# Performance work log

Measured on AMD Instinct MI355X. Metric: run time of the kernel, lower is better.

Reference implementation:

```python
import jax, jax.numpy as jnp
import numpy as np

K = 3
PAD = 1


def conv2d(x, w, b, pad):
    y = jax.lax.conv_general_dilated(
        x, w, window_strides=(1, 1), padding=[(pad, pad), (pad, pad)],
        dimension_numbers=("NCHW", "OIHW", "NCHW"))
    return y + b[None, :, None, None]


def dcn_v2(f, w_off, b_off, w, b):
    # Modulated deformable conv (DCNv2), stride=1, pad=1, dilation=1, dg=1.
    B, C, H, W = f.shape
    om = conv2d(f, w_off, b_off, PAD)                 # [B, 27, H, W]
    o1, o2, m = jnp.split(om, 3, axis=1)
    offset = jnp.concatenate([o1, o2], axis=1).reshape(B, K * K, 2, H, W)
    dy, dx = offset[:, :, 0], offset[:, :, 1]          # [B, 9, H, W]
    mask = jax.nn.sigmoid(m)                           # [B, 9, H, W]
    ky = (jnp.arange(K * K) // K).astype(f.dtype)      # kernel row per tap
    kx = (jnp.arange(K * K) % K).astype(f.dtype)       # kernel col per tap
    hh = jnp.arange(H, dtype=f.dtype)
    ww = jnp.arange(W, dtype=f.dtype)
    ys = hh[None, None, :, None] - PAD + ky[None, :, None, None] + dy  # [B,9,H,W]
    xs = ww[None, None, None, :] - PAD + kx[None, :, None, None] + dx
    y0 = jnp.floor(ys)
    x0 = jnp.floor(xs)
    wy1 = ys - y0
    wx1 = xs - x0
    wy0 = 1.0 - wy1
    wx0 = 1.0 - wx1
    f_flat = f.reshape(B, C, H * W)

    def gather(yi, xi):
        valid = (yi >= 0) & (yi <= H - 1) & (xi >= 0) & (xi <= W - 1)
        yc = jnp.clip(yi, 0, H - 1).astype(jnp.int32)
        xc = jnp.clip(xi, 0, W - 1).astype(jnp.int32)
        idx = (yc * W + xc).reshape(B, 1, -1)          # [B,1,9*H*W]
        g = jnp.take_along_axis(f_flat, idx, axis=2).reshape(B, C, K * K, H, W)
        return g * valid.astype(f.dtype).reshape(B, 1, K * K, H, W)

    v = (gather(y0, x0) * (wy0 * wx0)[:, None]
         + gather(y0, x0 + 1) * (wy0 * wx1)[:, None]
         + gather(y0 + 1, x0) * (wy1 * wx0)[:, None]
         + gather(y0 + 1, x0 + 1) * (wy1 * wx1)[:, None])   # [B,C,9,H,W]
    v = v * mask[:, None]
    out = jnp.einsum("bckhw,ock->bohw", v, w.reshape(w.shape[0], C, K * K))
    return out + b[None, :, None, None]


def setup_inputs() -> dict:
    key = jax.random.key(0)
    ks = jax.random.split(key, 10)
    B, C, H, W = 2, 256, 128, 128
    s = 0.05
    return {
        "x": jax.random.normal(ks[0], (B, C, H, W), jnp.float32),
        "votes": jax.random.normal(ks[1], (B, C, H, W), jnp.float32),
        "w1": jax.random.normal(ks[2], (C, C, 3, 3), jnp.float32) * s,
        "b1": jnp.zeros((C,), jnp.float32),
        "w_off": jax.random.normal(ks[3], (27, C, 3, 3), jnp.float32) * 0.01,
        "b_off": jnp.zeros((27,), jnp.float32),
        "w_dcn": jax.random.normal(ks[4], (C, C, 3, 3), jnp.float32) * s,
        "b_dcn": jnp.zeros((C,), jnp.float32),
        "w2": jax.random.normal(ks[5], (C, C, 3, 3), jnp.float32) * s,
        "b2": jnp.zeros((C,), jnp.float32),
        "w3": jax.random.normal(ks[6], (C, C, 3, 3), jnp.float32) * s,
        "b3": jnp.zeros((C,), jnp.float32),
        "w4": jax.random.normal(ks[7], (2, C, 1, 1), jnp.float32) * s,
        "b4": jnp.zeros((2,), jnp.float32),
    }


def reference(x, votes, w1, b1, w_off, b_off, w_dcn, b_dcn, w2, b2, w3, b3, w4, b4):
    v = jax.nn.relu(votes)
    t = jax.nn.relu(conv2d(v, w1, b1, PAD))            # conv3x3 + relu
    t = jax.nn.relu(dcn_v2(t, w_off, b_off, w_dcn, b_dcn))  # DCN + relu
    t = conv2d(t, w2, b2, PAD)                         # conv3x3 (no relu)
    g = t * x                                          # gated by x
    h = jax.nn.relu(conv2d(g, w3, b3, PAD))            # conv3x3 + relu
    out = conv2d(h, w4, b4, 0)                         # 1x1 -> outplanes
    return out
```

## Files before the change

kernel.cpp:

```cpp
#include <hip/hip_runtime.h>
#include <math.h>

typedef short short8 __attribute__((ext_vector_type(8)));
typedef float f32x4 __attribute__((ext_vector_type(4)));
typedef unsigned int uint4v __attribute__((ext_vector_type(4)));
typedef unsigned short ushort_t;

__device__ inline ushort_t f2bf(float f) {
    unsigned u = __builtin_bit_cast(unsigned, f);
    u = (u + 0x7fffu + ((u >> 16) & 1u)) >> 16;
    return (ushort_t)u;
}
__device__ inline float bf2f(ushort_t u) {
    return __builtin_bit_cast(float, (unsigned)u << 16);
}
__device__ inline void gload_lds16(const ushort_t* g, short* l) {
    __builtin_amdgcn_global_load_lds((const __attribute__((address_space(1))) unsigned int*)g,
                                     (__attribute__((address_space(3))) unsigned int*)l, 16, 0, 0);
}

__global__ __launch_bounds__(256)
void zeroinit_kernel(ushort_t* zp) { zp[threadIdx.x] = 0; }

template<bool RELU>
__global__ __launch_bounds__(256)
void nhwc_cvt_kernel(const float* __restrict__ in, ushort_t* __restrict__ out) {
    __shared__ short s[64 * 66];
    const int tid = threadIdx.x;
    const int px0 = blockIdx.x * 64;
    const int ci0 = blockIdx.y * 64;
    const int b   = blockIdx.z;
    const float* inb = in + (size_t)b * 256 * 16384;
#pragma unroll
    for (int rep = 0; rep < 16; ++rep) {
        int cl = rep * 4 + (tid >> 6);
        int pl = tid & 63;
        float v = inb[(size_t)(ci0 + cl) * 16384 + px0 + pl];
        if (RELU) v = fmaxf(v, 0.f);
        s[pl * 66 + cl] = (short)f2bf(v);
    }
    __syncthreads();
    ushort_t* ob = out + (size_t)b * 16384 * 256;
#pragma unroll
    for (int rep = 0; rep < 2; ++rep) {
        int c = rep * 256 + tid;
        int pl = c >> 3;
        int cl = (c & 7) * 8;
        *(short8*)&ob[(size_t)(px0 + pl) * 256 + ci0 + cl] = *(const short8*)&s[pl * 66 + cl];
    }
}

__global__ __launch_bounds__(256)
void wpack_kernel(const float* __restrict__ w, ushort_t* __restrict__ wpk,
                  int COUT, int NF) {
    int T = blockIdx.x * 256 + threadIdx.x;
    int lane = T & 63;
    int rest = T >> 6;
    int n = rest % NF;
    int kstep = rest / NF;
    int t = kstep >> 3, cc = kstep & 7;
    int oc = n * 16 + (lane & 15);
    int kk = (lane >> 4) * 8;
    short8 sv;
#pragma unroll
    for (int j = 0; j < 8; ++j) {
        int ci = cc * 32 + kk + j;
        float val = (oc < COUT) ? w[((size_t)oc * 256 + ci) * 9 + t] : 0.f;
        sv[j] = (short)f2bf(val);
    }
    *(short8*)&wpk[(size_t)T * 8] = sv;
}

template<int OUTC, int EPI>
__global__ __launch_bounds__(512, 2)
void conv_mfma_kernel(const ushort_t* __restrict__ in, const ushort_t* __restrict__ wpk,
                      const float* __restrict__ bias, int coutReal,
                      const ushort_t* __restrict__ xin, ushort_t* __restrict__ outp,
                      const ushort_t* __restrict__ zp)
{
    constexpr int NF = OUTC / 16;
    constexpr int NN = (NF < 4) ? NF : 4;
    constexpr int PITCH = OUTC + 4;
    union SM { short a[2][256 * 32]; float e[32 * PITCH]; };
    __shared__ __align__(16) SM sm;

    const int tid  = threadIdx.x;
    const int lane = tid & 63;
    const int wv   = tid >> 6;
    const int hi   = lane >> 4;
    const int lo   = lane & 15;
    const int pxg  = wv & 1;
    const int wn   = wv >> 1;
    const int wnu  = __builtin_amdgcn_readfirstlane(wn);
    const int x0 = blockIdx.x * 32;
    const int y0 = blockIdx.y * 4;
    const int b  = blockIdx.z;
    const ushort_t* inb = in + (size_t)b * 16384 * 256;

    const ushort_t* sptr[2];
    int sstep[2];
#pragma unroll
    for (int r = 0; r < 2; ++r) {
        int g = r * 512 + tid;
        int px = g >> 2, slot = g & 3;
        int hy = px / 34, hx = px - hy * 34;
        int gy = y0 - 1 + hy, gx = x0 - 1 + hx;
        bool ok = (px < 204) && ((unsigned)gy < 128u) && ((unsigned)gx < 128u);
        int kk = (px ^ (px >> 2)) & 3;
        sptr[r] = ok ? (inb + (size_t)((gy << 7) + gx) * 256 + ((slot ^ kk) << 3))
                     : (zp + (slot << 3));
        sstep[r] = ok ? 32 : 0;
    }

    int pxh_base[4];
#pragma unroll
    for (int m = 0; m < 4; ++m)
        pxh_base[m] = (2 * pxg + (m >> 1)) * 34 + (m & 1) * 16 + lo;

    f32x4 acc[4][NN];
#pragma unroll
    for (int m = 0; m < 4; ++m)
#pragma unroll
        for (int n = 0; n < NN; ++n) acc[m][n] = (f32x4){0.f, 0.f, 0.f, 0.f};

#pragma unroll
    for (int r = 0; r < 2; ++r)
        gload_lds16(sptr[r], &sm.a[0][(r * 512 + wv * 64) * 8]);
    __syncthreads();

    for (int cc = 0; cc < 8; ++cc) {
        const int buf = cc & 1;
        if (cc < 7) {
#pragma unroll
            for (int r = 0; r < 2; ++r)
                gload_lds16(sptr[r] + (size_t)(cc + 1) * sstep[r],
                            &sm.a[buf ^ 1][(r * 512 + wv * 64) * 8]);
        }
        if (NF >= 4 || wnu == 0) {
#pragma unroll
            for (int t = 0; t < 9; ++t) {
                const int ky = t / 3, kx = t % 3;
                short8 bf[NN];
#pragma unroll
                for (int n = 0; n < NN; ++n)
                    bf[n] = *(const short8*)&wpk[((size_t)((t * 8 + cc) * NF + wnu * 4 + n) * 64 + lane) * 8];
                short8 af[4];
#pragma unroll
                for (int m = 0; m < 4; ++m) {
                    int ph = pxh_base[m] + ky * 34 + kx;
                    int off = ph * 32 + ((hi ^ ((ph ^ (ph >> 2)) & 3)) << 3);
                    af[m] = *(const short8*)&sm.a[buf][off];
                }
#pragma unroll
                for (int m = 0; m < 4; ++m)
#pragma unroll
                    for (int n = 0; n < NN; ++n)
                        acc[m][n] = __builtin_amdgcn_mfma_f32_16x16x32_bf16(af[m], bf[n], acc[m][n], 0, 0, 0);
            }
        }
        __syncthreads();
    }

    float br[NN];
#pragma unroll
    for (int n = 0; n < NN; ++n) {
        int oc = wn * 64 + n * 16 + lo;
        br[n] = (oc < coutReal) ? bias[oc] : 0.f;
    }
    const size_t obase = ((size_t)b * 16384 + (size_t)y0 * 128 + x0) * OUTC;
#pragma unroll
    for (int p = 0; p < 4; ++p) {
        if (pxg == (p >> 1) && (NF >= 4 || wnu == 0)) {
#pragma unroll
            for (int mm = 0; mm < 2; ++mm) {
                int m = (p & 1) * 2 + mm;
#pragma unroll
                for (int n = 0; n < NN; ++n)
#pragma unroll
                    for (int r = 0; r < 4; ++r) {
                        int col = mm * 16 + hi * 4 + r;
                        float v = acc[m][n][r] + br[n];
                        if (EPI == 1) v = fmaxf(v, 0.f);
                        sm.e[col * PITCH + wn * 64 + n * 16 + lo] = v;
                    }
            }
        }
        __syncthreads();
        constexpr int CHUNKS = 32 * OUTC / 8;
        for (int c = tid; c < CHUNKS; c += 512) {
            int col = c / (OUTC / 8);
            int ch = c % (OUTC / 8);
            f32x4 v0 = *(const f32x4*)&sm.e[col * PITCH + ch * 8];
            f32x4 v1 = *(const f32x4*)&sm.e[col * PITCH + ch * 8 + 4];
            size_t gidx = obase + ((size_t)p * 128 + col) * OUTC + ch * 8;
            if (EPI == 2) {
                uint4v xu = *(const uint4v*)&xin[gidx];
#pragma unroll
                for (int j = 0; j < 4; ++j) {
                    float xa = bf2f((ushort_t)(xu[j] & 0xffffu));
                    float xb = __builtin_bit_cast(float, xu[j] & 0xffff0000u);
                    if (j < 2) { v0[2 * j] *= xa; v0[2 * j + 1] *= xb; }
                    else       { v1[2 * (j - 2)] *= xa; v1[2 * (j - 2) + 1] *= xb; }
                }
            }
            short8 s;
#pragma unroll
            for (int j = 0; j < 4; ++j) s[j] = (short)f2bf(v0[j]);
#pragma unroll
            for (int j = 0; j < 4; ++j) s[4 + j] = (short)f2bf(v1[j]);
            *(short8*)&outp[gidx] = s;
        }
        __syncthreads();
    }
}

__device__ inline void corner8(uint4v u, float w, float* sv) {
#pragma unroll
    for (int j = 0; j < 4; ++j) {
        unsigned a = u[j];
        sv[2 * j]     = fmaf(w, __builtin_bit_cast(float, a << 16), sv[2 * j]);
        sv[2 * j + 1] = fmaf(w, __builtin_bit_cast(float, a & 0xffff0000u), sv[2 * j + 1]);
    }
}

__global__ __launch_bounds__(256, 2)
void dcn_mfma_kernel(const ushort_t* __restrict__ ft, const ushort_t* __restrict__ omt,
                     const ushort_t* __restrict__ wpk, const float* __restrict__ bias,
                     ushort_t* __restrict__ outp)
{
    union SM { short a[2][2][2048]; float e[16 * 264]; };
    __shared__ __align__(16) SM sm;

    const int tid  = threadIdx.x;
    const int lane = tid & 63;
    const int wv   = tid >> 6;
    const int hi   = lane >> 4;
    const int lo   = lane & 15;
    const int bid  = blockIdx.x;
    const int tile = (bid & 7) * 64 + (bid >> 3);
    const int b    = tile >> 8;
    const int rem  = tile & 255;
    const int y0   = (rem >> 3) * 4;
    const int x0   = (rem & 7) * 16;
    const ushort_t* fb = ft + (size_t)b * 16384 * 256;

    const int pxl = (wv << 4) | (lane >> 2);
    const int q   = lane & 3;

    float mw[9][4];
    unsigned mc[9];
    {
        const int py = y0 + (pxl >> 4), pxx = x0 + (pxl & 15);
        const ushort_t* omp = omt + ((size_t)b * 16384 + py * 128 + pxx) * 32;
        uint4v ow[4];
#pragma unroll
        for (int j = 0; j < 4; ++j) ow[j] = *(const uint4v*)(omp + j * 8);
        unsigned wbuf[14];
#pragma unroll
        for (int j = 0; j < 4; ++j)
#pragma unroll
            for (int e = 0; e < 4; ++e)
                if (j * 4 + e < 14) wbuf[j * 4 + e] = ow[j][e];
#pragma unroll
        for (int t = 0; t < 9; ++t) {
            float dy = bf2f((ushort_t)(wbuf[t] & 0xffffu));
            float dx = bf2f((ushort_t)(wbuf[t] >> 16));
            unsigned mw_ = wbuf[(18 + t) >> 1];
            float mr = ((18 + t) & 1) ? bf2f((ushort_t)(mw_ >> 16)) : bf2f((ushort_t)(mw_ & 0xffffu));
            float mk = 1.f / (1.f + expf(-mr));
            float ys = (float)(py - 1 + t / 3) + dy;
            float xs = (float)(pxx - 1 + t % 3) + dx;
            float y0f = floorf(ys), x0f = floorf(xs);
            float wy1 = ys - y0f, wx1 = xs - x0f;
            float wy0 = 1.f - wy1, wx0 = 1.f - wx1;
            int yi = (int)y0f, xi = (int)x0f;
            bool vy0 = (yi >= 0) && (yi < 128), vy1 = (yi + 1 >= 0) && (yi + 1 < 128);
            bool vx0 = (xi >= 0) && (xi < 128), vx1 = (xi + 1 >= 0) && (xi + 1 < 128);
            mw[t][0] = (vy0 && vx0) ? wy0 * wx0 * mk : 0.f;
            mw[t][1] = (vy0 && vx1) ? wy0 * wx1 * mk : 0.f;
            mw[t][2] = (vy1 && vx0) ? wy1 * wx0 * mk : 0.f;
            mw[t][3] = (vy1 && vx1) ? wy1 * wx1 * mk : 0.f;
            int y0c = min(max(yi, 0), 127), y1c = min(max(yi + 1, 0), 127);
            int x0c = min(max(xi, 0), 127), x1c = min(max(xi + 1, 0), 127);
            mc[t] = (unsigned)y0c | ((unsigned)y1c << 8) | ((unsigned)x0c << 16) | ((unsigned)x1c << 24);
        }
    }

    const int w_off = pxl * 32 + ((q ^ ((pxl ^ (pxl >> 2)) & 3)) << 3);
    int a_off[4];
#pragma unroll
    for (int m = 0; m < 4; ++m) {
        int p_ = m * 16 + lo;
        a_off[m] = p_ * 32 + ((hi ^ ((p_ ^ (p_ >> 2)) & 3)) << 3);
    }

    f32x4 acc[4][4];
#pragma unroll
    for (int m = 0; m < 4; ++m)
#pragma unroll
        for (int n = 0; n < 4; ++n) acc[m][n] = (f32x4){0.f, 0.f, 0.f, 0.f};

    uint4v n0a, n0b, n0c, n0d;
    uint4v n1a, n1b, n1c, n1d;

    {
        unsigned c = mc[0];
        int yy0 = c & 255, yy1 = (c >> 8) & 255, xx0 = (c >> 16) & 255, xx1 = c >> 24;
        size_t o00 = (size_t)((yy0 << 7) + xx0) * 256, o01 = (size_t)((yy0 << 7) + xx1) * 256;
        size_t o10 = (size_t)((yy1 << 7) + xx0) * 256, o11 = (size_t)((yy1 << 7) + xx1) * 256;
#pragma unroll
        for (int h = 0; h < 2; ++h) {
            const ushort_t* pc = fb + h * 32 + q * 8;
            uint4v g0 = *(const uint4v*)(pc + o00);
            uint4v g1 = *(const uint4v*)(pc + o01);
            uint4v g2 = *(const uint4v*)(pc + o10);
            uint4v g3 = *(const uint4v*)(pc + o11);
            float sv[8] = {0.f, 0.f, 0.f, 0.f, 0.f, 0.f, 0.f, 0.f};
            corner8(g0, mw[0][0], sv); corner8(g1, mw[0][1], sv);
            corner8(g2, mw[0][2], sv); corner8(g3, mw[0][3], sv);
            unsigned pk[4];
#pragma unroll
            for (int j = 0; j < 4; ++j)
                asm("v_cvt_pk_bf16_f32 %0, %1, %2" : "=v"(pk[j]) : "v"(sv[2 * j]), "v"(sv[2 * j + 1]));
            *(uint4v*)&sm.a[0][h][w_off] = (uint4v){pk[0], pk[1], pk[2], pk[3]};
        }
    }
    __syncthreads();

    for (int cch = 0; cch < 4; ++cch) {
#pragma unroll
        for (int t = 0; t < 9; ++t) {
            const int cur = (cch + t) & 1;
            const bool last = (cch == 3) && (t == 8);
            const int tn   = (t == 8) ? 0 : t + 1;
            const int cchn = (t == 8) ? cch + 1 : cch;
            if (!last) {
                unsigned c = mc[tn];
                int yy0 = c & 255, yy1 = (c >> 8) & 255, xx0 = (c >> 16) & 255, xx1 = c >> 24;
                size_t o00 = (size_t)((yy0 << 7) + xx0) * 256, o01 = (size_t)((yy0 << 7) + xx1) * 256;
                size_t o10 = (size_t)((yy1 << 7) + xx0) * 256, o11 = (size_t)((yy1 << 7) + xx1) * 256;
                const ushort_t* pc0 = fb + (2 * cchn) * 32 + q * 8;
                n0a = *(const uint4v*)(pc0 + o00);
                n0b = *(const uint4v*)(pc0 + o01);
                n0c = *(const uint4v*)(pc0 + o10);
                n0d = *(const uint4v*)(pc0 + o11);
                const ushort_t* pc1 = pc0 + 32;
                n1a = *(const uint4v*)(pc1 + o00);
                n1b = *(const uint4v*)(pc1 + o01);
                n1c = *(const uint4v*)(pc1 + o10);
                n1d = *(const uint4v*)(pc1 + o11);
            }
            short8 bfr0[4], bfr1[4];
            {
                const ushort_t* bs0 = wpk + ((size_t)((t * 8 + 2 * cch) * 16 + wv * 4) * 64 + lane) * 8;
#pragma unroll
                for (int n = 0; n < 4; ++n)
                    bfr0[n] = *(const short8*)(bs0 + (size_t)n * 512);
                const ushort_t* bs1 = bs0 + 16 * 512;
#pragma unroll
                for (int n = 0; n < 4; ++n)
                    bfr1[n] = *(const short8*)(bs1 + (size_t)n * 512);
            }
#pragma unroll
            for (int m = 0; m < 4; ++m) {
                short8 af0 = *(const short8*)&sm.a[cur][0][a_off[m]];
                short8 af1 = *(const short8*)&sm.a[cur][1][a_off[m]];
#pragma unroll
                for (int n = 0; n < 4; ++n)
                    acc[m][n] = __builtin_amdgcn_mfma_f32_16x16x32_bf16(af0, bfr0[n], acc[m][n], 0, 0, 0);
#pragma unroll
                for (int n = 0; n < 4; ++n)
                    acc[m][n] = __builtin_amdgcn_mfma_f32_16x16x32_bf16(af1, bfr1[n], acc[m][n], 0, 0, 0);
            }
            if (!last) {
                {
                    float sv[8] = {0.f, 0.f, 0.f, 0.f, 0.f, 0.f, 0.f, 0.f};
                    corner8(n0a, mw[tn][0], sv); corner8(n0b, mw[tn][1], sv);
                    corner8(n0c, mw[tn][2], sv); corner8(n0d, mw[tn][3], sv);
                    unsigned pk[4];
#pragma unroll
                    for (int j = 0; j < 4; ++j)
                        asm("v_cvt_pk_bf16_f32 %0, %1, %2" : "=v"(pk[j]) : "v"(sv[2 * j]), "v"(sv[2 * j + 1]));
                    *(uint4v*)&sm.a[cur ^ 1][0][w_off] = (uint4v){pk[0], pk[1], pk[2], pk[3]};
                }
                {
                    float sv[8] = {0.f, 0.f, 0.f, 0.f, 0.f, 0.f, 0.f, 0.f};
                    corner8(n1a, mw[tn][0], sv); corner8(n1b, mw[tn][1], sv);
                    corner8(n1c, mw[tn][2], sv); corner8(n1d, mw[tn][3], sv);
                    unsigned pk[4];
#pragma unroll
                    for (int j = 0; j < 4; ++j)
                        asm("v_cvt_pk_bf16_f32 %0, %1, %2" : "=v"(pk[j]) : "v"(sv[2 * j]), "v"(sv[2 * j + 1]));
                    *(uint4v*)&sm.a[cur ^ 1][1][w_off] = (uint4v){pk[0], pk[1], pk[2], pk[3]};
                }
            }
            __syncthreads();
        }
    }

    float br[4];
#pragma unroll
    for (int n = 0; n < 4; ++n) br[n] = bias[wv * 64 + n * 16 + lo];
#pragma unroll
    for (int p = 0; p < 4; ++p) {
#pragma unroll
        for (int n = 0; n < 4; ++n)
#pragma unroll
            for (int r = 0; r < 4; ++r)
                sm.e[(hi * 4 + r) * 264 + wv * 64 + n * 16 + lo] = fmaxf(acc[p][n][r] + br[n], 0.f);
        __syncthreads();
#pragma unroll
        for (int j = 0; j < 2; ++j) {
            int c2 = j * 256 + tid;
            int pl = c2 >> 5, ch = c2 & 31;
            f32x4 v0 = *(const f32x4*)&sm.e[pl * 264 + ch * 8];
            f32x4 v1 = *(const f32x4*)&sm.e[pl * 264 + ch * 8 + 4];
            short8 s;
#pragma unroll
            for (int jj = 0; jj < 4; ++jj) s[jj] = (short)f2bf(v0[jj]);
#pragma unroll
            for (int jj = 0; jj < 4; ++jj) s[4 + jj] = (short)f2bf(v1[jj]);
            *(short8*)&outp[((size_t)b * 16384 + (size_t)(y0 + p) * 128 + x0 + pl) * 256 + ch * 8] = s;
        }
        __syncthreads();
    }
}

__global__ __launch_bounds__(256)
void conv1x1_kernel(const ushort_t* __restrict__ in, const float* __restrict__ w,
                    const float* __restrict__ bias, float* __restrict__ out)
{
    __shared__ float sw[512];
    for (int i = threadIdx.x; i < 512; i += 256) sw[i] = w[i];
    __syncthreads();
    int px = blockIdx.x * 256 + threadIdx.x;
    int b = px >> 14, p = px & 16383;
    const ushort_t* ip = in + (size_t)px * 256;
    float a0 = 0.f, a1 = 0.f;
#pragma unroll
    for (int ch = 0; ch < 32; ++ch) {
        uint4v u = *(const uint4v*)&ip[ch * 8];
#pragma unroll
        for (int j = 0; j < 4; ++j) {
            int ci = ch * 8 + 2 * j;
            float fa = __builtin_bit_cast(float, u[j] << 16);
            float fb = __builtin_bit_cast(float, u[j] & 0xffff0000u);
            a0 = fmaf(fa, sw[ci], a0);      a1 = fmaf(fa, sw[256 + ci], a1);
            a0 = fmaf(fb, sw[ci + 1], a0);  a1 = fmaf(fb, sw[256 + ci + 1], a1);
        }
    }
    out[(size_t)b * 2 * 16384 + p]         = a0 + bias[0];
    out[(size_t)b * 2 * 16384 + 16384 + p] = a1 + bias[1];
}

extern "C" void kernel_launch(void* const* d_in, const int* in_sizes, int n_in,
                              void* d_out, int out_size, void* d_ws, size_t ws_size,
                              hipStream_t stream) {
    const float* x     = (const float*)d_in[0];
    const float* votes = (const float*)d_in[1];
    const float* w1    = (const float*)d_in[2];
    const float* b1    = (const float*)d_in[3];
    const float* w_off = (const float*)d_in[4];
    const float* b_off = (const float*)d_in[5];
    const float* w_dcn = (const float*)d_in[6];
    const float* b_dcn = (const float*)d_in[7];
    const float* w2    = (const float*)d_in[8];
    const float* b2    = (const float*)d_in[9];
    const float* w3    = (const float*)d_in[10];
    const float* b3    = (const float*)d_in[11];
    const float* w4    = (const float*)d_in[12];
    const float* b4    = (const float*)d_in[13];
    float* outp = (float*)d_out;

    const int B = 2;
    const size_t featN = (size_t)B * 16384 * 256;

    ushort_t* ws   = (ushort_t*)d_ws;
    ushort_t* t1   = ws;
    ushort_t* t2   = t1 + featN;
    ushort_t* aN   = t2 + featN;
    ushort_t* xN   = aN + featN;
    ushort_t* om   = xN + featN;
    ushort_t* wpk1 = om + (size_t)B * 16384 * 32;
    ushort_t* wpkO = wpk1 + 589824;
    ushort_t* wpkD = wpkO + 73728;
    ushort_t* wpk2 = wpkD + 589824;
    ushort_t* wpk3 = wpk2 + 589824;
    ushort_t* zp   = wpk3 + 589824;

    zeroinit_kernel<<<1, 256, 0, stream>>>(zp);
    nhwc_cvt_kernel<true><<<dim3(256, 4, B), 256, 0, stream>>>(votes, aN);
    nhwc_cvt_kernel<false><<<dim3(256, 4, B), 256, 0, stream>>>(x, xN);
    wpack_kernel<<<288, 256, 0, stream>>>(w1, wpk1, 256, 16);
    wpack_kernel<<<36, 256, 0, stream>>>(w_off, wpkO, 27, 2);
    wpack_kernel<<<288, 256, 0, stream>>>(w_dcn, wpkD, 256, 16);
    wpack_kernel<<<288, 256, 0, stream>>>(w2, wpk2, 256, 16);
    wpack_kernel<<<288, 256, 0, stream>>>(w3, wpk3, 256, 16);

    dim3 cg(4, 32, B);
    conv_mfma_kernel<256, 1><<<cg, 512, 0, stream>>>(aN, wpk1, b1, 256, nullptr, t1, zp);
    conv_mfma_kernel<32, 0><<<cg, 512, 0, stream>>>(t1, wpkO, b_off, 27, nullptr, om, zp);
    dcn_mfma_kernel<<<512, 256, 0, stream>>>(t1, om, wpkD, b_dcn, t2);
    conv_mfma_kernel<256, 2><<<cg, 512, 0, stream>>>(t2, wpk2, b2, 256, xN, aN, zp);
    conv_mfma_kernel<256, 1><<<cg, 512, 0, stream>>>(aN, wpk3, b3, 256, nullptr, xN, zp);
    conv1x1_kernel<<<128, 256, 0, stream>>>(xN, w4, b4, outp);
}
```

Baseline: 278.0 us.

## Split conv output channels across blocks and merge prep kernels

The 3x3 conv kernels now compute 128 output channels per block, with the channel half picked from blockIdx.z. This doubles the grid from 256 to 512 blocks and halves the accumulator count per wave (NN 4 to 2). The weight-pack, zero-init and NHWC conversion launches are merged into two kernels to cut launch overhead. In exchange, each input tile is loaded into LDS twice, once per channel half, and each block issues fewer MFMAs per A-fragment load.

```diff
diff --git a/kernel.cpp b/kernel.cpp
--- a/kernel.cpp
+++ b/kernel.cpp
@@ -19,41 +19,9 @@
                                      (__attribute__((address_space(3))) unsigned int*)l, 16, 0, 0);
 }
 
-__global__ __launch_bounds__(256)
-void zeroinit_kernel(ushort_t* zp) { zp[threadIdx.x] = 0; }
-
-template<bool RELU>
-__global__ __launch_bounds__(256)
-void nhwc_cvt_kernel(const float* __restrict__ in, ushort_t* __restrict__ out) {
-    __shared__ short s[64 * 66];
-    const int tid = threadIdx.x;
-    const int px0 = blockIdx.x * 64;
-    const int ci0 = blockIdx.y * 64;
-    const int b   = blockIdx.z;
-    const float* inb = in + (size_t)b * 256 * 16384;
-#pragma unroll
-    for (int rep = 0; rep < 16; ++rep) {
-        int cl = rep * 4 + (tid >> 6);
-        int pl = tid & 63;
-        float v = inb[(size_t)(ci0 + cl) * 16384 + px0 + pl];
-        if (RELU) v = fmaxf(v, 0.f);
-        s[pl * 66 + cl] = (short)f2bf(v);
-    }
-    __syncthreads();
-    ushort_t* ob = out + (size_t)b * 16384 * 256;
-#pragma unroll
-    for (int rep = 0; rep < 2; ++rep) {
-        int c = rep * 256 + tid;
-        int pl = c >> 3;
-        int cl = (c & 7) * 8;
-        *(short8*)&ob[(size_t)(px0 + pl) * 256 + ci0 + cl] = *(const short8*)&s[pl * 66 + cl];
-    }
-}
-
-__global__ __launch_bounds__(256)
-void wpack_kernel(const float* __restrict__ w, ushort_t* __restrict__ wpk,
-                  int COUT, int NF) {
-    int T = blockIdx.x * 256 + threadIdx.x;
+__device__ inline void wpack_body(const float* __restrict__ w, ushort_t* __restrict__ wpk,
+                                  int COUT, int NF, int bidLocal, int tid) {
+    int T = bidLocal * 256 + tid;
     int lane = T & 63;
     int rest = T >> 6;
     int n = rest % NF;
@@ -71,15 +39,61 @@
     *(short8*)&wpk[(size_t)T * 8] = sv;
 }
 
+__global__ __launch_bounds__(256)
+void wpack_all_kernel(const float* w1, ushort_t* wpk1,
+                      const float* w_off, ushort_t* wpkO,
+                      const float* w_dcn, ushort_t* wpkD,
+                      const float* w2, ushort_t* wpk2,
+                      const float* w3, ushort_t* wpk3,
+                      ushort_t* zp) {
+    int bid = blockIdx.x, tid = threadIdx.x;
+    if (bid < 288)       wpack_body(w1,    wpk1, 256, 16, bid,        tid);
+    else if (bid < 324)  wpack_body(w_off, wpkO, 27,  2,  bid - 288,  tid);
+    else if (bid < 612)  wpack_body(w_dcn, wpkD, 256, 16, bid - 324,  tid);
+    else if (bid < 900)  wpack_body(w2,    wpk2, 256, 16, bid - 612,  tid);
+    else if (bid < 1188) wpack_body(w3,    wpk3, 256, 16, bid - 900,  tid);
+    else                 zp[tid] = 0;
+}
+
+__global__ __launch_bounds__(256)
+void nhwc_all_kernel(const float* __restrict__ votes, const float* __restrict__ x,
+                     ushort_t* __restrict__ aN, ushort_t* __restrict__ xN) {
+    __shared__ short s[64 * 66];
+    const int tid = threadIdx.x;
+    const int px0 = blockIdx.x * 64;
+    const int ci0 = blockIdx.y * 64;
+    const int z   = blockIdx.z;
+    const int b   = z & 1;
+    const bool doRelu = (z < 2);
+    const float* inb = (doRelu ? votes : x) + (size_t)b * 256 * 16384;
+    ushort_t* ob = (doRelu ? aN : xN) + (size_t)b * 16384 * 256;
+#pragma unroll
+    for (int rep = 0; rep < 16; ++rep) {
+        int cl = rep * 4 + (tid >> 6);
+        int pl = tid & 63;
+        float v = inb[(size_t)(ci0 + cl) * 16384 + px0 + pl];
+        if (doRelu) v = fmaxf(v, 0.f);
+        s[pl * 66 + cl] = (short)f2bf(v);
+    }
+    __syncthreads();
+#pragma unroll
+    for (int rep = 0; rep < 2; ++rep) {
+        int c = rep * 256 + tid;
+        int pl = c >> 3;
+        int cl = (c & 7) * 8;
+        *(short8*)&ob[(size_t)(px0 + pl) * 256 + ci0 + cl] = *(const short8*)&s[pl * 66 + cl];
+    }
+}
+
 template<int OUTC, int EPI>
 __global__ __launch_bounds__(512, 2)
 void conv_mfma_kernel(const ushort_t* __restrict__ in, const ushort_t* __restrict__ wpk,
                       const float* __restrict__ bias, int coutReal,
                       const ushort_t* __restrict__ xin, ushort_t* __restrict__ outp,
-                      const ushort_t* __restrict__ zp)
+                      const ushort_t* __restrict__ zp, int nfTot, int nOcBlk, int ocStr)
 {
     constexpr int NF = OUTC / 16;
-    constexpr int NN = (NF < 4) ? NF : 4;
+    constexpr int NN = (NF < 4) ? NF : NF / 4;
     constexpr int PITCH = OUTC + 4;
     union SM { short a[2][256 * 32]; float e[32 * PITCH]; };
     __shared__ __align__(16) SM sm;
@@ -92,9 +106,11 @@
     const int pxg  = wv & 1;
     const int wn   = wv >> 1;
     const int wnu  = __builtin_amdgcn_readfirstlane(wn);
+    const int bz   = blockIdx.z;
+    const int ocblk = bz % nOcBlk;
+    const int b    = bz / nOcBlk;
     const int x0 = blockIdx.x * 32;
     const int y0 = blockIdx.y * 4;
-    const int b  = blockIdx.z;
     const ushort_t* inb = in + (size_t)b * 16384 * 256;
 
     const ushort_t* sptr[2];
@@ -143,7 +159,7 @@
                 short8 bf[NN];
 #pragma unroll
                 for (int n = 0; n < NN; ++n)
-                    bf[n] = *(const short8*)&wpk[((size_t)((t * 8 + cc) * NF + wnu * 4 + n) * 64 + lane) * 8];
+                    bf[n] = *(const short8*)&wpk[((size_t)((t * 8 + cc) * nfTot + ocblk * NF + wnu * NN + n) * 64 + lane) * 8];
                 short8 af[4];
 #pragma unroll
                 for (int m = 0; m < 4; ++m) {
@@ -164,10 +180,10 @@
     float br[NN];
 #pragma unroll
     for (int n = 0; n < NN; ++n) {
-        int oc = wn * 64 + n * 16 + lo;
+        int oc = ocblk * OUTC + wn * (16 * NN) + n * 16 + lo;
         br[n] = (oc < coutReal) ? bias[oc] : 0.f;
     }
-    const size_t obase = ((size_t)b * 16384 + (size_t)y0 * 128 + x0) * OUTC;
+    const size_t obase = ((size_t)b * 16384 + (size_t)y0 * 128 + x0) * ocStr;
 #pragma unroll
     for (int p = 0; p < 4; ++p) {
         if (pxg == (p >> 1) && (NF >= 4 || wnu == 0)) {
@@ -181,7 +197,7 @@
                         int col = mm * 16 + hi * 4 + r;
                         float v = acc[m][n][r] + br[n];
                         if (EPI == 1) v = fmaxf(v, 0.f);
-                        sm.e[col * PITCH + wn * 64 + n * 16 + lo] = v;
+                        sm.e[col * PITCH + wn * (16 * NN) + n * 16 + lo] = v;
                     }
             }
         }
@@ -192,7 +208,7 @@
             int ch = c % (OUTC / 8);
             f32x4 v0 = *(const f32x4*)&sm.e[col * PITCH + ch * 8];
             f32x4 v1 = *(const f32x4*)&sm.e[col * PITCH + ch * 8 + 4];
-            size_t gidx = obase + ((size_t)p * 128 + col) * OUTC + ch * 8;
+            size_t gidx = obase + ((size_t)p * 128 + col) * ocStr + ocblk * OUTC + ch * 8;
             if (EPI == 2) {
                 uint4v xu = *(const uint4v*)&xin[gidx];
 #pragma unroll
@@ -488,20 +504,16 @@
     ushort_t* wpk3 = wpk2 + 589824;
     ushort_t* zp   = wpk3 + 589824;
 
-    zeroinit_kernel<<<1, 256, 0, stream>>>(zp);
-    nhwc_cvt_kernel<true><<<dim3(256, 4, B), 256, 0, stream>>>(votes, aN);
-    nhwc_cvt_kernel<false><<<dim3(256, 4, B), 256, 0, stream>>>(x, xN);
-    wpack_kernel<<<288, 256, 0, stream>>>(w1, wpk1, 256, 16);
-    wpack_kernel<<<36, 256, 0, stream>>>(w_off, wpkO, 27, 2);
-    wpack_kernel<<<288, 256, 0, stream>>>(w_dcn, wpkD, 256, 16);
-    wpack_kernel<<<288, 256, 0, stream>>>(w2, wpk2, 256, 16);
-    wpack_kernel<<<288, 256, 0, stream>>>(w3, wpk3, 256, 16);
-
-    dim3 cg(4, 32, B);
-    conv_mfma_kernel<256, 1><<<cg, 512, 0, stream>>>(aN, wpk1, b1, 256, nullptr, t1, zp);
-    conv_mfma_kernel<32, 0><<<cg, 512, 0, stream>>>(t1, wpkO, b_off, 27, nullptr, om, zp);
+    wpack_all_kernel<<<1189, 256, 0, stream>>>(w1, wpk1, w_off, wpkO, w_dcn, wpkD,
+                                               w2, wpk2, w3, wpk3, zp);
+    nhwc_all_kernel<<<dim3(256, 4, 4), 256, 0, stream>>>(votes, x, aN, xN);
+
+    dim3 cgS(4, 32, B * 2);
+    dim3 cgO(4, 32, B);
+    conv_mfma_kernel<128, 1><<<cgS, 512, 0, stream>>>(aN, wpk1, b1, 256, nullptr, t1, zp, 16, 2, 256);
+    conv_mfma_kernel<32, 0><<<cgO, 512, 0, stream>>>(t1, wpkO, b_off, 27, nullptr, om, zp, 2, 1, 32);
     dcn_mfma_kernel<<<512, 256, 0, stream>>>(t1, om, wpkD, b_dcn, t2);
-    conv_mfma_kernel<256, 2><<<cg, 512, 0, stream>>>(t2, wpk2, b2, 256, xN, aN, zp);
-    conv_mfma_kernel<256, 1><<<cg, 512, 0, stream>>>(aN, wpk3, b3, 256, nullptr, xN, zp);
+    conv_mfma_kernel<128, 2><<<cgS, 512, 0, stream>>>(t2, wpk2, b2, 256, xN, aN, zp, 16, 2, 256);
+    conv_mfma_kernel<128, 1><<<cgS, 512, 0, stream>>>(aN, wpk3, b3, 256, nullptr, xN, zp, 16, 2, 256);
     conv1x1_kernel<<<128, 256, 0, stream>>>(xN, w4, b4, outp);
 }
```

Result: slower. 306.1 us (+10.1%).
